# Optimization experiments

Hardware: AMD Instinct MI355X
Metric: run time of the kernel (lower is better)

The kernel has to match this reference:

```python
import jax, jax.numpy as jnp
import numpy as np

K = 7          # involution kernel size
PAD = (K - 1) // 2
C = 256        # channels
GC = 16        # group_channels (hardcoded in module)
G = C // GC    # groups = 16
RED = C // 4   # reduction channels = 64
EPS = 1e-5


def _bn_eval(x, gamma, beta, mean, var):
    # eval-mode BatchNorm2d over channel dim of NCHW
    inv = gamma / jnp.sqrt(var + EPS)
    return x * inv[None, :, None, None] + (beta - mean * inv)[None, :, None, None]


def setup_inputs() -> dict:
    key = jax.random.key(0)
    ks = jax.random.split(key, 12)
    x = jax.random.normal(ks[0], (8, C, 56, 56), dtype=jnp.float32)
    # conv1: 1x1, C -> C/4, no bias (followed by BN+ReLU)
    w1 = jax.random.normal(ks[1], (RED, C), dtype=jnp.float32) * (1.0 / np.sqrt(C))
    bn1_gamma = 1.0 + 0.1 * jax.random.normal(ks[2], (RED,), dtype=jnp.float32)
    bn1_beta = 0.1 * jax.random.normal(ks[3], (RED,), dtype=jnp.float32)
    bn1_mean = 0.1 * jax.random.normal(ks[4], (RED,), dtype=jnp.float32)
    bn1_var = jax.random.uniform(ks[5], (RED,), dtype=jnp.float32, minval=0.5, maxval=1.5)
    # conv2: 1x1, C/4 -> K^2 * groups, with bias, no BN/act
    w2 = jax.random.normal(ks[6], (K * K * G, RED), dtype=jnp.float32) * (1.0 / np.sqrt(RED))
    b2 = 0.1 * jax.random.normal(ks[7], (K * K * G,), dtype=jnp.float32)
    # final BN on output channels
    bn2_gamma = 1.0 + 0.1 * jax.random.normal(ks[8], (C,), dtype=jnp.float32)
    bn2_beta = 0.1 * jax.random.normal(ks[9], (C,), dtype=jnp.float32)
    bn2_mean = 0.1 * jax.random.normal(ks[10], (C,), dtype=jnp.float32)
    bn2_var = jax.random.uniform(ks[11], (C,), dtype=jnp.float32, minval=0.5, maxval=1.5)
    return {
        "x": x, "w1": w1,
        "bn1_gamma": bn1_gamma, "bn1_beta": bn1_beta, "bn1_mean": bn1_mean, "bn1_var": bn1_var,
        "w2": w2, "b2": b2,
        "bn2_gamma": bn2_gamma, "bn2_beta": bn2_beta, "bn2_mean": bn2_mean, "bn2_var": bn2_var,
    }


def reference(x, w1, bn1_gamma, bn1_beta, bn1_mean, bn1_var,
              w2, b2, bn2_gamma, bn2_beta, bn2_mean, bn2_var):
    b, c, h, w = x.shape
    # --- kernel generation branch (stride == 1, no avgpool) ---
    t = jnp.einsum('bchw,oc->bohw', x, w1)            # [b, RED, h, w]
    t = jax.nn.relu(_bn_eval(t, bn1_gamma, bn1_beta, bn1_mean, bn1_var))
    wgt = jnp.einsum('bchw,oc->bohw', t, w2) + b2[None, :, None, None]  # [b, K^2*G, h, w]
    wgt = wgt.reshape(b, G, K * K, h, w)
    # --- unfold: patches ordered (c, kh, kw) to match nn.Unfold ---
    xp = jnp.pad(x, ((0, 0), (0, 0), (PAD, PAD), (PAD, PAD)))
    patches = jnp.stack(
        [xp[:, :, i:i + h, j:j + w] for i in range(K) for j in range(K)],
        axis=2,
    )  # [b, c, K^2, h, w]
    patches = patches.reshape(b, G, GC, K * K, h, w)
    # --- per-pixel multiply-sum over kernel footprint ---
    out = jnp.einsum('bgkhw,bgckhw->bgchw', wgt, patches).reshape(b, c, h, w)
    out = jax.nn.relu(_bn_eval(out, bn2_gamma, bn2_beta, bn2_mean, bn2_var))
    return out
```

## Files before the change

kernel.cpp:

```cpp
#include <hip/hip_runtime.h>
#include <hip/hip_fp16.h>

#define NB   8
#define NC   256
#define HW   56
#define NPX  3136
#define RED  64
#define NG   16
#define GC   16
#define KS   7
#define KK   49
#define PADK 3
#define XPH  62
#define XPW  64
#define XPSLICE (XPH * XPW)
#define TPX  224
#define NT2  14
#define XT2_CS 644
#define WSTR2  232

typedef float f32x4 __attribute__((ext_vector_type(4)));
typedef _Float16 h16x4 __attribute__((ext_vector_type(4)));
typedef _Float16 h16x8 __attribute__((ext_vector_type(8)));

__global__ __launch_bounds__(256) void prep_kernel(
    const float* __restrict__ x, const float* __restrict__ w1,
    const float* __restrict__ w2, _Float16* __restrict__ xpad,
    _Float16* __restrict__ w1h, _Float16* __restrict__ w2h) {
    int bid = blockIdx.x;
    if (bid < NB * NC) {
        int b = bid & 7, c = bid >> 3;
        const float* xs = x + ((size_t)b * NC + c) * NPX;
        _Float16* xd = xpad + ((size_t)b * NC + c) * XPSLICE;
#pragma unroll 4
        for (int e = threadIdx.x; e < XPSLICE; e += 256) {
            int row = e >> 6, col = e & 63;
            int h = row - PADK, w = col - PADK;
            float v = (h >= 0 && h < HW && w >= 0 && w < HW) ? xs[h * HW + w] : 0.0f;
            xd[e] = (_Float16)v;
        }
    } else if (bid < NB * NC + NG) {
        int g = bid - NB * NC;
#pragma unroll 4
        for (int e = threadIdx.x; e < 4096; e += 256) {
            int m = e >> 6, k = e & 63;
            float v = (m < KK) ? w2[((size_t)g * KK + m) * RED + k] : 0.0f;
            w2h[(size_t)g * 4096 + e] = (_Float16)v;
        }
    } else {
#pragma unroll 4
        for (int e = threadIdx.x; e < 64 * 256; e += 256)
            w1h[e] = (_Float16)w1[e];
    }
}

__global__ __launch_bounds__(64) void conv1_kernel(
    const _Float16* __restrict__ xpad, const _Float16* __restrict__ w1h,
    const float* __restrict__ g1, const float* __restrict__ be1,
    const float* __restrict__ mu1, const float* __restrict__ var1,
    _Float16* __restrict__ tT) {
    int lane = threadIdx.x;
    int l15 = lane & 15, l4 = lane >> 4;
    int wgid = blockIdx.x;
    int b  = wgid & 7;
    int nt = wgid >> 3;
    int px = nt * 16 + l15;
    int h = px / HW, w = px % HW;

    const _Float16* xp = xpad + (size_t)b * NC * XPSLICE
                       + (h + PADK) * XPW + (w + PADK);

    f32x4 acc0 = {0,0,0,0}, acc1 = {0,0,0,0}, acc2 = {0,0,0,0}, acc3 = {0,0,0,0};
#pragma unroll
    for (int kk = 0; kk < 8; ++kk) {
        h16x8 bfr;
#pragma unroll
        for (int i = 0; i < 8; ++i)
            bfr[i] = xp[(size_t)(kk * 32 + l4 * 8 + i) * XPSLICE];
#pragma unroll
        for (int mt = 0; mt < 4; ++mt) {
            const _Float16* ap = w1h + (mt * 16 + l15) * NC + kk * 32 + l4 * 8;
            h16x8 a = *(const h16x8*)ap;
            f32x4 c = (mt == 0) ? acc0 : (mt == 1) ? acc1 : (mt == 2) ? acc2 : acc3;
            c = __builtin_amdgcn_mfma_f32_16x16x32_f16(a, bfr, c, 0, 0, 0);
            if (mt == 0) acc0 = c; else if (mt == 1) acc1 = c;
            else if (mt == 2) acc2 = c; else acc3 = c;
        }
    }

    _Float16* tb = tT + ((size_t)b * NPX + px) * RED;
#pragma unroll
    for (int mt = 0; mt < 4; ++mt) {
        f32x4 a = (mt == 0) ? acc0 : (mt == 1) ? acc1 : (mt == 2) ? acc2 : acc3;
        int o0 = mt * 16 + l4 * 4;
        h16x4 pk;
#pragma unroll
        for (int r = 0; r < 4; ++r) {
            int o = o0 + r;
            float inv = g1[o] * rsqrtf(var1[o] + 1e-5f);
            float v = a[r] * inv + (be1[o] - mu1[o] * inv);
            pk[r] = (_Float16)fmaxf(v, 0.0f);
        }
        *(h16x4*)(tb + o0) = pk;
    }
}

__global__ __launch_bounds__(448, 3) void involution_kernel(
    const _Float16* __restrict__ xpad, const _Float16* __restrict__ tT,
    const _Float16* __restrict__ w2h, const float* __restrict__ b2,
    const float* __restrict__ g2, const float* __restrict__ be2,
    const float* __restrict__ mu2, const float* __restrict__ var2,
    float* __restrict__ out) {
    __shared__ __align__(16) _Float16 xtap[GC * XT2_CS];
    __shared__ __align__(16) _Float16 wls[KK * WSTR2];

    int tid  = threadIdx.x;
    int lane = tid & 63;
    int wv   = __builtin_amdgcn_readfirstlane(tid >> 6);
    int wgid = blockIdx.x;
    int swz  = (wgid & 7) * 224 + (wgid >> 3);
    int b    = swz / 224;
    int rem  = swz % 224;
    int g    = rem / NT2;
    int tile = rem % NT2;
    int px0 = tile * TPX;
    int R0  = tile * 4;

    const _Float16* xpg = xpad + ((size_t)b * NC + (size_t)g * GC) * XPSLICE;

    h16x8 xr[3];
#pragma unroll
    for (int u = 0; u < 3; ++u) {
        int cid = u * 448 + tid;
        if (cid < 1280) {
            int ch = cid / 80;
            int rm = cid % 80;
            int rr = rm >> 3, c8 = rm & 7;
            xr[u] = *(const h16x8*)(xpg + (size_t)ch * XPSLICE
                                    + (R0 + rr) * XPW + c8 * 8);
        }
    }

    {
        int l15 = lane & 15, l4 = lane >> 4;
        const _Float16* wA = w2h + (size_t)g * 4096;
        const float* bg = b2 + (size_t)g * KK;
        h16x8 a0[4], a1[4];
#pragma unroll
        for (int mt = 0; mt < 4; ++mt) {
            const _Float16* ap = wA + (mt * 16 + l15) * 64 + l4 * 8;
            a0[mt] = *(const h16x8*)(ap);
            a1[mt] = *(const h16x8*)(ap + 32);
        }
#pragma unroll
        for (int it = 0; it < 2; ++it) {
            int nt = wv * 2 + it;
            int pxc = px0 + nt * 16 + l15;
            const _Float16* tp = tT + ((size_t)b * NPX + pxc) * RED + l4 * 8;
            h16x8 bfr0 = *(const h16x8*)tp;
            h16x8 bfr1 = *(const h16x8*)(tp + 32);

            f32x4 acc0 = {0,0,0,0}, acc1 = {0,0,0,0},
                  acc2 = {0,0,0,0}, acc3 = {0,0,0,0};
#pragma unroll
            for (int mt = 0; mt < 4; ++mt) {
                f32x4 a = (mt == 0) ? acc0 : (mt == 1) ? acc1
                        : (mt == 2) ? acc2 : acc3;
                a = __builtin_amdgcn_mfma_f32_16x16x32_f16(a0[mt], bfr0, a, 0, 0, 0);
                a = __builtin_amdgcn_mfma_f32_16x16x32_f16(a1[mt], bfr1, a, 0, 0, 0);
                if (mt == 0) acc0 = a; else if (mt == 1) acc1 = a;
                else if (mt == 2) acc2 = a; else acc3 = a;
            }
            _Float16* wl = wls + nt * 16 + l15;
#pragma unroll
            for (int mt = 0; mt < 4; ++mt) {
                f32x4 a = (mt == 0) ? acc0 : (mt == 1) ? acc1
                        : (mt == 2) ? acc2 : acc3;
#pragma unroll
                for (int r = 0; r < 4; ++r) {
                    int k = mt * 16 + l4 * 4 + r;
                    if (k < KK) wl[k * WSTR2] = (_Float16)(a[r] + bg[k]);
                }
            }
        }
    }

#pragma unroll
    for (int u = 0; u < 3; ++u) {
        int cid = u * 448 + tid;
        if (cid < 1280) {
            int ch = cid / 80;
            int rm = cid % 80;
            int rr = rm >> 3, c8 = rm & 7;
            *(h16x8*)&xtap[ch * XT2_CS + rr * 64 + c8 * 8] = xr[u];
        }
    }
    __syncthreads();

    int octet = tid >> 4;
    int ch    = tid & 15;
    int lin   = octet * 8;
    int lh    = lin / 56;
    int w0    = lin % 56;

    const _Float16* xb0 = xtap + ch * XT2_CS + lh * 64 + w0;
    float acc[8];
#pragma unroll
    for (int p = 0; p < 8; ++p) acc[p] = 0.0f;

#pragma unroll
    for (int i = 0; i < KS; ++i) {
        h16x8 t0 = *(const h16x8*)(xb0 + i * 64);
        h16x8 t1 = *(const h16x8*)(xb0 + i * 64 + 8);
        float cc[16];
#pragma unroll
        for (int p = 0; p < 8; ++p) { cc[p] = (float)t0[p]; cc[8 + p] = (float)t1[p]; }
#pragma unroll
        for (int j = 0; j < KS; ++j) {
            h16x8 wq = *(const h16x8*)&wls[(i * KS + j) * WSTR2 + lin];
#pragma unroll
            for (int p = 0; p < 8; ++p)
                acc[p] = fmaf((float)wq[p], cc[j + p], acc[p]);
        }
    }

    int c_ = g * GC + ch;
    float inv = g2[c_] * rsqrtf(var2[c_] + 1e-5f);
    float off = be2[c_] - mu2[c_] * inv;
    float* op = out + ((size_t)b * NC + c_) * NPX + px0 + lin;
    f32x4 o0, o1;
#pragma unroll
    for (int p = 0; p < 4; ++p) {
        o0[p] = fmaxf(acc[p] * inv + off, 0.0f);
        o1[p] = fmaxf(acc[4 + p] * inv + off, 0.0f);
    }
    *(f32x4*)(op)     = o0;
    *(f32x4*)(op + 4) = o1;
}

extern "C" void kernel_launch(void* const* d_in, const int* in_sizes, int n_in,
                              void* d_out, int out_size, void* d_ws, size_t ws_size,
                              hipStream_t stream) {
    const float* x    = (const float*)d_in[0];
    const float* w1   = (const float*)d_in[1];
    const float* g1   = (const float*)d_in[2];
    const float* be1  = (const float*)d_in[3];
    const float* mu1  = (const float*)d_in[4];
    const float* var1 = (const float*)d_in[5];
    const float* w2   = (const float*)d_in[6];
    const float* b2   = (const float*)d_in[7];
    const float* g2   = (const float*)d_in[8];
    const float* be2  = (const float*)d_in[9];
    const float* mu2  = (const float*)d_in[10];
    const float* var2 = (const float*)d_in[11];
    float* outp = (float*)d_out;

    _Float16* xpad = (_Float16*)d_ws;
    _Float16* tT   = xpad + (size_t)NB * NC * XPSLICE;
    _Float16* w2h  = tT + (size_t)NB * NPX * RED;
    _Float16* w1h  = w2h + (size_t)NG * 4096;

    prep_kernel<<<NB * NC + NG + 1, 256, 0, stream>>>(x, w1, w2, xpad, w1h, w2h);
    conv1_kernel<<<1568, 64, 0, stream>>>(xpad, w1h, g1, be1, mu1, var1, tT);
    involution_kernel<<<1792, 448, 0, stream>>>(
        xpad, tT, w2h, b2, g2, be2, mu2, var2, outp);
}
```

Before: 63.94 us.

## Fuse fp16 padded-input conversion into conv1, prep only zeroes borders

The prep kernel no longer converts the full input to a padded fp16 buffer; it only writes zeros into the padding border. conv1 now reads the fp32 input directly, converts it to fp16 for its MFMA operand, and writes the interior of the padded fp16 buffer as a side effect. This removes one full read of the fp16 padded tensor and a separate pass over the input. The cost is that conv1 now reads fp32 with a strided per-channel pattern and does scattered 2-byte stores, which may coalesce poorly.

```diff
diff --git a/kernel.cpp b/kernel.cpp
--- a/kernel.cpp
+++ b/kernel.cpp
@@ -24,20 +24,21 @@
 typedef _Float16 h16x8 __attribute__((ext_vector_type(8)));
 
 __global__ __launch_bounds__(256) void prep_kernel(
-    const float* __restrict__ x, const float* __restrict__ w1,
-    const float* __restrict__ w2, _Float16* __restrict__ xpad,
-    _Float16* __restrict__ w1h, _Float16* __restrict__ w2h) {
+    const float* __restrict__ w1, const float* __restrict__ w2,
+    _Float16* __restrict__ xpad, _Float16* __restrict__ w1h,
+    _Float16* __restrict__ w2h) {
     int bid = blockIdx.x;
     if (bid < NB * NC) {
         int b = bid & 7, c = bid >> 3;
-        const float* xs = x + ((size_t)b * NC + c) * NPX;
         _Float16* xd = xpad + ((size_t)b * NC + c) * XPSLICE;
-#pragma unroll 4
-        for (int e = threadIdx.x; e < XPSLICE; e += 256) {
-            int row = e >> 6, col = e & 63;
-            int h = row - PADK, w = col - PADK;
-            float v = (h >= 0 && h < HW && w >= 0 && w < HW) ? xs[h * HW + w] : 0.0f;
-            xd[e] = (_Float16)v;
+#pragma unroll
+        for (int e = threadIdx.x; e < 832; e += 256) {
+            int row, col;
+            if (e < 192)      { row = e >> 6;              col = e & 63; }
+            else if (e < 384) { int f = e - 192; row = 59 + (f >> 6); col = f & 63; }
+            else              { int f = e - 384; row = 3 + (f >> 3);
+                                int c8 = f & 7;  col = (c8 < 3) ? c8 : 56 + c8; }
+            xd[row * XPW + col] = (_Float16)0.0f;
         }
     } else if (bid < NB * NC + NG) {
         int g = bid - NB * NC;
@@ -55,10 +56,10 @@
 }
 
 __global__ __launch_bounds__(64) void conv1_kernel(
-    const _Float16* __restrict__ xpad, const _Float16* __restrict__ w1h,
+    const float* __restrict__ x, const _Float16* __restrict__ w1h,
     const float* __restrict__ g1, const float* __restrict__ be1,
     const float* __restrict__ mu1, const float* __restrict__ var1,
-    _Float16* __restrict__ tT) {
+    _Float16* __restrict__ tT, _Float16* __restrict__ xpad) {
     int lane = threadIdx.x;
     int l15 = lane & 15, l4 = lane >> 4;
     int wgid = blockIdx.x;
@@ -67,8 +68,9 @@
     int px = nt * 16 + l15;
     int h = px / HW, w = px % HW;
 
-    const _Float16* xp = xpad + (size_t)b * NC * XPSLICE
-                       + (h + PADK) * XPW + (w + PADK);
+    const float* xp = x + (size_t)b * NC * NPX + px;
+    _Float16* xpw = xpad + (size_t)b * NC * XPSLICE
+                  + (h + PADK) * XPW + (w + PADK);
 
     f32x4 acc0 = {0,0,0,0}, acc1 = {0,0,0,0}, acc2 = {0,0,0,0}, acc3 = {0,0,0,0};
 #pragma unroll
@@ -76,7 +78,10 @@
         h16x8 bfr;
 #pragma unroll
         for (int i = 0; i < 8; ++i)
-            bfr[i] = xp[(size_t)(kk * 32 + l4 * 8 + i) * XPSLICE];
+            bfr[i] = (_Float16)xp[(size_t)(kk * 32 + l4 * 8 + i) * NPX];
+#pragma unroll
+        for (int i = 0; i < 8; ++i)
+            xpw[(size_t)(kk * 32 + l4 * 8 + i) * XPSLICE] = bfr[i];
 #pragma unroll
         for (int mt = 0; mt < 4; ++mt) {
             const _Float16* ap = w1h + (mt * 16 + l15) * NC + kk * 32 + l4 * 8;
@@ -260,8 +265,8 @@
     _Float16* w2h  = tT + (size_t)NB * NPX * RED;
     _Float16* w1h  = w2h + (size_t)NG * 4096;
 
-    prep_kernel<<<NB * NC + NG + 1, 256, 0, stream>>>(x, w1, w2, xpad, w1h, w2h);
-    conv1_kernel<<<1568, 64, 0, stream>>>(xpad, w1h, g1, be1, mu1, var1, tT);
+    prep_kernel<<<NB * NC + NG + 1, 256, 0, stream>>>(w1, w2, xpad, w1h, w2h);
+    conv1_kernel<<<1568, 64, 0, stream>>>(x, w1h, g1, be1, mu1, var1, tT, xpad);
     involution_kernel<<<1792, 448, 0, stream>>>(
         xpad, tT, w2h, b2, g2, be2, mu2, var2, outp);
 }
```

New measurement: 64.44 us. Within noise of the previous version (+0.8%).
